# Kernel optimization log

Hardware: AMD Instinct MI355X
Metric: run time of the kernel (lower is better)

The kernel has to match this reference:

```python
import jax, jax.numpy as jnp
import numpy as np

N_HEADS = 16
D_EMBED = 1024
BATCH = 1
SEQ = 4096


def setup_inputs() -> dict:
    key = jax.random.key(0)
    ks = jax.random.split(key, 5)
    d = D_EMBED
    x = jax.random.normal(ks[0], (BATCH, SEQ, d), dtype=jnp.float32)
    # torch Linear weights stored as (in, out) so y = x @ W + b
    W_in = jax.random.normal(ks[1], (d, 3 * d), dtype=jnp.float32) / np.sqrt(d)
    b_in = jax.random.normal(ks[2], (3 * d,), dtype=jnp.float32) * 0.02
    W_out = jax.random.normal(ks[3], (d, d), dtype=jnp.float32) / np.sqrt(d)
    b_out = jax.random.normal(ks[4], (d,), dtype=jnp.float32) * 0.02
    return {"x": x, "W_in": W_in, "b_in": b_in, "W_out": W_out, "b_out": b_out}


def reference(x, W_in, b_in, W_out, b_out):
    B, S, d = x.shape
    H = N_HEADS
    dh = d // H
    qkv = x @ W_in + b_in                      # [B, S, 3d]
    q, k, v = jnp.split(qkv, 3, axis=-1)       # each [B, S, d]
    # [B, S, H, dh] -> [B, H, S, dh]
    q = q.reshape(B, S, H, dh).transpose(0, 2, 1, 3)
    k = k.reshape(B, S, H, dh).transpose(0, 2, 1, 3)
    v = v.reshape(B, S, H, dh).transpose(0, 2, 1, 3)
    scores = jnp.einsum("bhqd,bhkd->bhqk", q, k) / jnp.sqrt(jnp.float32(dh))
    causal = jnp.tril(jnp.ones((S, S), dtype=bool))  # True = keep
    scores = jnp.where(causal, scores, -jnp.inf)
    attn = jax.nn.softmax(scores, axis=-1)
    out = jnp.einsum("bhqk,bhkd->bhqd", attn, v)     # [B, H, S, dh]
    out = out.transpose(0, 2, 1, 3).reshape(B, S, d)
    return out @ W_out + b_out
```

## Files before the change

kernel.cpp:

```cpp
#include <hip/hip_runtime.h>
#include <stdint.h>

#define S_LEN 4096
#define D_EMB 1024
#define NH 16
#define DHEAD 64
#define N3 3072

typedef __attribute__((ext_vector_type(8))) short short8;
typedef __attribute__((ext_vector_type(4))) short short4v;
typedef __attribute__((ext_vector_type(4))) float f32x4;

#define OFF_XB    0u
#define OFF_WINT  4194304u
#define OFF_WOUTT 7340032u
#define OFF_Q     8388608u
#define OFF_ATTN  20971520u

#define QSCALE 0.1803368801111204f
#define DEFER_THR 11.0f

__device__ __forceinline__ unsigned short f2bf(float f) {
  unsigned u = __float_as_uint(f);
  unsigned r = u + 0x7FFFu + ((u >> 16) & 1u);
  return (unsigned short)(r >> 16);
}
__device__ __forceinline__ unsigned cvtpk_bf16(float lo, float hi) {
  unsigned r;
  asm("v_cvt_pk_bf16_f32 %0, %1, %2" : "=v"(r) : "v"(lo), "v"(hi));
  return r;
}
__device__ __forceinline__ void gload16(const void* g, void* l) {
  __builtin_amdgcn_global_load_lds((const __attribute__((address_space(1))) void*)g,
                                   (__attribute__((address_space(3))) void*)l, 16, 0, 0);
}

__global__ __launch_bounds__(256) void prep_kernel(const float* __restrict__ x,
                                                   const float* __restrict__ W_in,
                                                   const float* __restrict__ W_out,
                                                   ushort* __restrict__ xb,
                                                   ushort* __restrict__ wint,
                                                   ushort* __restrict__ woutt) {
  __shared__ float tile[32][65];
  int b = blockIdx.x;
  int tid = threadIdx.x;
  if (b < 4096) {
    int i = (b * 256 + tid) * 4;
    float4 v = *(const float4*)(x + i);
    ushort4 o;
    o.x = f2bf(v.x); o.y = f2bf(v.y); o.z = f2bf(v.z); o.w = f2bf(v.w);
    *(ushort4*)(xb + i) = o;
    return;
  }
  const float* src;
  ushort* dst;
  int C, bx, by;
  if (b < 5632) {
    int t = b - 4096;
    src = W_in; dst = wint; C = N3;
    bx = t % 48; by = t / 48;
  } else {
    int t = b - 5632;
    src = W_out; dst = woutt; C = D_EMB;
    bx = t & 15; by = t >> 4;
  }
  const int R = D_EMB;
  int r0 = by * 32, c0 = bx * 64;
  int lr = tid >> 3, lc8 = (tid & 7) * 8;
  float4 v0 = *(const float4*)&src[(size_t)(r0 + lr) * C + c0 + lc8];
  float4 v1 = *(const float4*)&src[(size_t)(r0 + lr) * C + c0 + lc8 + 4];
  tile[lr][lc8 + 0] = v0.x; tile[lr][lc8 + 1] = v0.y;
  tile[lr][lc8 + 2] = v0.z; tile[lr][lc8 + 3] = v0.w;
  tile[lr][lc8 + 4] = v1.x; tile[lr][lc8 + 5] = v1.y;
  tile[lr][lc8 + 6] = v1.z; tile[lr][lc8 + 7] = v1.w;
  __syncthreads();
  int oc = tid >> 2, q = tid & 3;
  short8 o;
#pragma unroll
  for (int i = 0; i < 8; ++i) o[i] = (short)f2bf(tile[q * 8 + i][oc]);
  *(short8*)&dst[(size_t)(c0 + oc) * R + r0 + q * 8] = o;
}

__global__ __launch_bounds__(512, 2) void gemm1_8phase(const ushort* __restrict__ A,
                                                       const ushort* __restrict__ Bt,
                                                       const float* __restrict__ bias,
                                                       ushort* __restrict__ o16) {
  __shared__ ushort L[57344];
  const int K = 1024;
  int tid = threadIdx.x, w = tid >> 6, lane = tid & 63;
  int wr = w >> 2, wc = w & 3;
  int l15 = lane & 15, g = lane >> 4;
  int lr = lane >> 3, lc = lane & 7;
  int swcol = (lc ^ lr) * 8;
  int rxor = (l15 & 7) << 3;
  int id = blockIdx.y * 16 + blockIdx.x;
  int id2 = (id & 7) * 32 + (id >> 3);
  int bm = (id2 >> 4) * 256, bn = (id2 & 15) * 192;

  f32x4 acc[8][3];
#pragma unroll
  for (int m = 0; m < 8; ++m)
#pragma unroll
    for (int n = 0; n < 3; ++n) acc[m][n] = (f32x4){0.f, 0.f, 0.f, 0.f};

  auto stageA = [&](int t, int h) {
#pragma unroll
    for (int r2 = 0; r2 < 2; ++r2)
      gload16(A + (size_t)(bm + h * 128 + r2 * 64 + w * 8 + lr) * K + t * 64 + swcol,
              &L[(t & 1) * 16384 + h * 8192 + r2 * 4096 + w * 512]);
  };
  auto stageB0 = [&](int t) {
#pragma unroll
    for (int r2 = 0; r2 < 2; ++r2)
      gload16(Bt + (size_t)(bn + r2 * 64 + w * 8 + lr) * K + t * 64 + swcol,
              &L[32768 + (t & 1) * 12288 + r2 * 4096 + w * 512]);
  };
  auto stageB1 = [&](int t) {
    gload16(Bt + (size_t)(bn + 128 + w * 8 + lr) * K + t * 64 + swcol,
            &L[32768 + (t & 1) * 12288 + 8192 + w * 512]);
  };

  short8 bf[3][2], af[2][2];
  auto readB = [&](int tb) {
    int base = 32768 + tb * 12288;
#pragma unroll
    for (int n = 0; n < 3; ++n)
#pragma unroll
      for (int ks = 0; ks < 2; ++ks)
        bf[n][ks] = *(const short8*)&L[base + (wc * 48 + n * 16 + l15) * 64 + ((ks * 32 + g * 8) ^ rxor)];
  };
  auto readA2 = [&](int tb, int m0) {
    int base = tb * 16384 + wr * 8192;
#pragma unroll
    for (int mi = 0; mi < 2; ++mi)
#pragma unroll
      for (int ks = 0; ks < 2; ++ks)
        af[mi][ks] = *(const short8*)&L[base + ((m0 + mi) * 16 + l15) * 64 + ((ks * 32 + g * 8) ^ rxor)];
  };
  auto mfma6 = [&](int m0) {
#pragma unroll
    for (int mi = 0; mi < 2; ++mi)
#pragma unroll
      for (int n = 0; n < 3; ++n)
#pragma unroll
        for (int ks = 0; ks < 2; ++ks)
          acc[m0 + mi][n] =
              __builtin_amdgcn_mfma_f32_16x16x32_bf16(af[mi][ks], bf[n][ks], acc[m0 + mi][n], 0, 0, 0);
  };

#define BAR() __builtin_amdgcn_s_barrier()
#define LGK0() asm volatile("s_waitcnt lgkmcnt(0)" ::: "memory")
#define VM3() asm volatile("s_waitcnt vmcnt(3)" ::: "memory")
#define VM0() asm volatile("s_waitcnt vmcnt(0)" ::: "memory")

  stageA(0, 0); stageA(0, 1); stageB0(0); stageB1(0);
  stageB0(1); stageB1(1);
  VM3();
  BAR();

  for (int i = 0; i < 8; ++i) {
    int T = 2 * i;
    bool more = (T + 2 < 16);
    readB(0); readA2(0, 0); stageA(T + 1, 0);
    BAR(); LGK0();
    __builtin_amdgcn_s_setprio(1); mfma6(0); __builtin_amdgcn_s_setprio(0);
    BAR();
    readA2(0, 2); stageA(T + 1, 1);
    BAR(); LGK0();
    __builtin_amdgcn_s_setprio(1); mfma6(2); __builtin_amdgcn_s_setprio(0);
    BAR();
    readA2(0, 4); if (more) stageB0(T + 2);
    BAR(); LGK0();
    __builtin_amdgcn_s_setprio(1); mfma6(4); __builtin_amdgcn_s_setprio(0);
    BAR();
    readA2(0, 6); if (more) stageB1(T + 2);
    BAR(); LGK0();
    __builtin_amdgcn_s_setprio(1); mfma6(6); __builtin_amdgcn_s_setprio(0);
    if (more) VM3(); else VM0();
    BAR();
    readB(1); readA2(1, 0); if (more) stageA(T + 2, 0);
    BAR(); LGK0();
    __builtin_amdgcn_s_setprio(1); mfma6(0); __builtin_amdgcn_s_setprio(0);
    BAR();
    readA2(1, 2); if (more) stageA(T + 2, 1);
    BAR(); LGK0();
    __builtin_amdgcn_s_setprio(1); mfma6(2); __builtin_amdgcn_s_setprio(0);
    BAR();
    readA2(1, 4); if (more) stageB0(T + 3);
    BAR(); LGK0();
    __builtin_amdgcn_s_setprio(1); mfma6(4); __builtin_amdgcn_s_setprio(0);
    BAR();
    readA2(1, 6); if (more) stageB1(T + 3);
    BAR(); LGK0();
    __builtin_amdgcn_s_setprio(1); mfma6(6); __builtin_amdgcn_s_setprio(0);
    if (more) VM3(); else VM0();
    BAR();
  }
#undef BAR
#undef LGK0
#undef VM3
#undef VM0

#pragma unroll
  for (int m = 0; m < 8; ++m) {
    int rbase = bm + wr * 128 + m * 16 + g * 4;
#pragma unroll
    for (int n = 0; n < 3; ++n) {
      int c = bn + wc * 48 + n * 16 + l15;
      float bv = bias[c];
      int which = c >> 10, cc = c & 1023, hh = cc >> 6, dcol = cc & 63;
      if (which == 2) {
        ushort4 o;
        o.x = f2bf(acc[m][n][0] + bv);
        o.y = f2bf(acc[m][n][1] + bv);
        o.z = f2bf(acc[m][n][2] + bv);
        o.w = f2bf(acc[m][n][3] + bv);
        *(ushort4*)&o16[8388608u + (size_t)hh * (DHEAD * (size_t)S_LEN) +
                        (size_t)dcol * S_LEN + rbase] = o;
      } else {
        float qs = (which == 0) ? QSCALE : 1.0f;
        ushort* dst = o16 + (size_t)which * 4194304u +
                      (size_t)hh * (S_LEN * DHEAD) + dcol;
#pragma unroll
        for (int j = 0; j < 4; ++j)
          dst[(size_t)(rbase + j) * DHEAD] = f2bf((acc[m][n][j] + bv) * qs);
      }
    }
  }
}

#define BK 64

__global__ __launch_bounds__(256) void gemm2_kernel(const ushort* __restrict__ A,
                                                    const ushort* __restrict__ Bt,
                                                    const float* __restrict__ bias,
                                                    float* __restrict__ o32,
                                                    int N, int K) {
  __shared__ ushort L[36864];
  int tid = threadIdx.x, w = tid >> 6, lane = tid & 63;
  int wr = w >> 1, wc = w & 1;
  int l15 = lane & 15, g = lane >> 4;
  int lr = lane >> 3, lc = lane & 7;
  int swcol = (lc ^ lr) * 8;
  int rxor = (l15 & 7) << 3;
  int gx = gridDim.x;
  int id = blockIdx.y * gx + blockIdx.x;
  int q8 = (gx * gridDim.y) >> 3;
  int id2 = (id & 7) * q8 + (id >> 3);
  int bm = (id2 / gx) * 128, bn = (id2 % gx) * 64;
  f32x4 acc[4][2];
#pragma unroll
  for (int m = 0; m < 4; ++m)
#pragma unroll
    for (int n = 0; n < 2; ++n) acc[m][n] = (f32x4){0.f, 0.f, 0.f, 0.f};

  auto stage = [&](int t) {
    int buf = t % 3;
#pragma unroll
    for (int i = 0; i < 4; ++i) {
      int ch = w * 4 + i;
      gload16(A + (size_t)(bm + ch * 8 + lr) * K + t * 64 + swcol,
              &L[buf * 8192 + ch * 512]);
    }
#pragma unroll
    for (int i = 0; i < 2; ++i) {
      int ch = w * 2 + i;
      gload16(Bt + (size_t)(bn + ch * 8 + lr) * K + t * 64 + swcol,
              &L[24576 + buf * 4096 + ch * 512]);
    }
  };

  const int NT = 16;
  stage(0); stage(1);
  asm volatile("s_waitcnt vmcnt(6)" ::: "memory");
  __builtin_amdgcn_s_barrier();

  for (int t = 0; t < NT; ++t) {
    int buf = t % 3;
    if (t + 2 < NT) stage(t + 2);
    const ushort* Ab = &L[buf * 8192];
    const ushort* Bb = &L[24576 + buf * 4096];
    short8 a[4][2], b[2][2];
#pragma unroll
    for (int m = 0; m < 4; ++m)
#pragma unroll
      for (int ks = 0; ks < 2; ++ks)
        a[m][ks] = *(const short8*)&Ab[(wr * 64 + m * 16 + l15) * 64 + ((ks * 32 + g * 8) ^ rxor)];
#pragma unroll
    for (int n = 0; n < 2; ++n)
#pragma unroll
      for (int ks = 0; ks < 2; ++ks)
        b[n][ks] = *(const short8*)&Bb[(wc * 32 + n * 16 + l15) * 64 + ((ks * 32 + g * 8) ^ rxor)];
    asm volatile("s_waitcnt lgkmcnt(0)" ::: "memory");
    __builtin_amdgcn_s_setprio(1);
#pragma unroll
    for (int m = 0; m < 4; ++m)
#pragma unroll
      for (int n = 0; n < 2; ++n)
#pragma unroll
        for (int ks = 0; ks < 2; ++ks)
          acc[m][n] = __builtin_amdgcn_mfma_f32_16x16x32_bf16(a[m][ks], b[n][ks], acc[m][n], 0, 0, 0);
    __builtin_amdgcn_s_setprio(0);
    if (t + 2 < NT)
      asm volatile("s_waitcnt vmcnt(6)" ::: "memory");
    else if (t + 1 < NT)
      asm volatile("s_waitcnt vmcnt(0)" ::: "memory");
    __builtin_amdgcn_s_barrier();
  }

#pragma unroll
  for (int m = 0; m < 4; ++m) {
    int rbase = bm + wr * 64 + m * 16 + g * 4;
#pragma unroll
    for (int n = 0; n < 2; ++n) {
      int c = bn + wc * 32 + n * 16 + l15;
      float bv = bias[c];
#pragma unroll
      for (int j = 0; j < 4; ++j)
        o32[(size_t)(rbase + j) * N + c] = acc[m][n][j] + bv;
    }
  }
}

__global__ __launch_bounds__(512) void attn_kernel(const ushort* __restrict__ Q,
                                                   const ushort* __restrict__ Kg,
                                                   const ushort* __restrict__ Vtg,
                                                   ushort* __restrict__ O) {
  __shared__ ushort Ks[2][64 * 64];
  __shared__ ushort Vs[2][64 * 64];
  int bid = blockIdx.x;
  int h = bid & 15;
  int qt = (bid < 256) ? (31 - (bid >> 4)) : ((bid - 256) >> 4);
  int q0 = qt * 128;
  int tid = threadIdx.x, w = tid >> 6, lane = tid & 63;
  int l15 = lane & 15, g = lane >> 4;
  const ushort* qh = Q + (size_t)h * (S_LEN * DHEAD);
  const ushort* kh = Kg + (size_t)h * (S_LEN * DHEAD);
  const ushort* vh = Vtg + (size_t)h * (DHEAD * (size_t)S_LEN);
  int srow = w * 8 + (lane >> 3);
  int sgcol = (((lane & 7) ^ ((lane >> 3) & 7))) * 8;
  ushort* kdst0 = &Ks[0][w * 512];  ushort* kdst1 = &Ks[1][w * 512];
  ushort* vdst0 = &Vs[0][w * 512];  ushort* vdst1 = &Vs[1][w * 512];
  int kxor = (l15 & 7) << 4;
  int koff0 = ((g * 16) ^ kxor) >> 1;
  int koff1 = ((64 + g * 16) ^ kxor) >> 1;
  int voff[4];
#pragma unroll
  for (int ct = 0; ct < 4; ++ct) voff[ct] = ((ct * 32 + g * 8) ^ kxor) >> 1;

  int qrow = q0 + w * 16 + l15;
  short8 aq[2];
#pragma unroll
  for (int t = 0; t < 2; ++t)
    aq[t] = *(const short8*)&qh[(size_t)qrow * DHEAD + t * 32 + g * 8];

  f32x4 acc_o[4];
#pragma unroll
  for (int dt = 0; dt < 4; ++dt) acc_o[dt] = (f32x4){0.f, 0.f, 0.f, 0.f};
  float m = -1e30f, l = 0.f;
  int last = 2 * qt + 1;

  gload16(&kh[(size_t)srow * DHEAD + sgcol], kdst0);
  gload16(&vh[(size_t)srow * S_LEN + sgcol], vdst0);
  asm volatile("s_waitcnt vmcnt(0)" ::: "memory");
  __syncthreads();
  int cur = 0;

  for (int it = 0; it <= last; ++it) {
    int kv0 = it * 64;
    bool more = (it < last);
    const ushort* Kc = Ks[cur];
    const ushort* Vc = Vs[cur];

    if (more) {
      int kv1 = kv0 + 64;
      gload16(&kh[(size_t)(kv1 + srow) * DHEAD + sgcol], cur ? kdst0 : kdst1);
      gload16(&vh[(size_t)srow * S_LEN + kv1 + sgcol], cur ? vdst0 : vdst1);
    }

    f32x4 accs[4];
#pragma unroll
    for (int ct = 0; ct < 4; ++ct) accs[ct] = (f32x4){0.f, 0.f, 0.f, 0.f};
    __builtin_amdgcn_s_setprio(1);
#pragma unroll
    for (int ct = 0; ct < 4; ++ct) {
      int rb = (ct * 16 + l15) * 64;
      short8 kf0 = *(const short8*)&Kc[rb + koff0];
      short8 kf1 = *(const short8*)&Kc[rb + koff1];
      accs[ct] = __builtin_amdgcn_mfma_f32_16x16x32_bf16(kf0, aq[0], accs[ct], 0, 0, 0);
      accs[ct] = __builtin_amdgcn_mfma_f32_16x16x32_bf16(kf1, aq[1], accs[ct], 0, 0, 0);
    }
    __builtin_amdgcn_s_setprio(0);

    if (it >= 2 * qt) {
#pragma unroll
      for (int ct = 0; ct < 4; ++ct) {
        int kbase = kv0 + ct * 16 + g * 4;
#pragma unroll
        for (int j = 0; j < 4; ++j)
          if (kbase + j > qrow) accs[ct][j] = -1e30f;
      }
    }

    float a0 = fmaxf(fmaxf(accs[0][0], accs[0][1]), fmaxf(accs[0][2], accs[0][3]));
    float a1 = fmaxf(fmaxf(accs[1][0], accs[1][1]), fmaxf(accs[1][2], accs[1][3]));
    float a2 = fmaxf(fmaxf(accs[2][0], accs[2][1]), fmaxf(accs[2][2], accs[2][3]));
    float a3 = fmaxf(fmaxf(accs[3][0], accs[3][1]), fmaxf(accs[3][2], accs[3][3]));
    float pm = fmaxf(fmaxf(a0, a1), fmaxf(a2, a3));

    if (!__all(pm <= m + DEFER_THR)) {
      pm = fmaxf(pm, __shfl_xor(pm, 16));
      pm = fmaxf(pm, __shfl_xor(pm, 32));
      float mnew = fmaxf(m, pm);
      float corr = __builtin_amdgcn_exp2f(m - mnew);
      l *= corr; m = mnew;
#pragma unroll
      for (int dt = 0; dt < 4; ++dt)
#pragma unroll
        for (int j = 0; j < 4; ++j) acc_o[dt][j] *= corr;
    }

    float rs = 0.f;
    short8 pk8[2];
#pragma unroll
    for (int t2 = 0; t2 < 2; ++t2) {
      float p0 = __builtin_amdgcn_exp2f(accs[2 * t2][0] - m);
      float p1 = __builtin_amdgcn_exp2f(accs[2 * t2][1] - m);
      float p2 = __builtin_amdgcn_exp2f(accs[2 * t2][2] - m);
      float p3 = __builtin_amdgcn_exp2f(accs[2 * t2][3] - m);
      float p4 = __builtin_amdgcn_exp2f(accs[2 * t2 + 1][0] - m);
      float p5 = __builtin_amdgcn_exp2f(accs[2 * t2 + 1][1] - m);
      float p6 = __builtin_amdgcn_exp2f(accs[2 * t2 + 1][2] - m);
      float p7 = __builtin_amdgcn_exp2f(accs[2 * t2 + 1][3] - m);
      rs += ((p0 + p1) + (p2 + p3)) + ((p4 + p5) + (p6 + p7));
      union { unsigned u[4]; short8 v; } pu;
      pu.u[0] = cvtpk_bf16(p0, p1);
      pu.u[1] = cvtpk_bf16(p2, p3);
      pu.u[2] = cvtpk_bf16(p4, p5);
      pu.u[3] = cvtpk_bf16(p6, p7);
      pk8[t2] = pu.v;
    }
    l += rs;

    __builtin_amdgcn_s_setprio(1);
#pragma unroll
    for (int dt = 0; dt < 4; ++dt) {
      int rb = (dt * 16 + l15) * 64;
#pragma unroll
      for (int t2 = 0; t2 < 2; ++t2) {
        union { short4v hh[2]; short8 v; } vu;
        vu.hh[0] = *(const short4v*)&Vc[rb + voff[2 * t2]];
        vu.hh[1] = *(const short4v*)&Vc[rb + voff[2 * t2 + 1]];
        acc_o[dt] = __builtin_amdgcn_mfma_f32_16x16x32_bf16(vu.v, pk8[t2], acc_o[dt], 0, 0, 0);
      }
    }
    __builtin_amdgcn_s_setprio(0);

    asm volatile("s_waitcnt vmcnt(0)" ::: "memory");
    __syncthreads();
    cur ^= 1;
  }

  l += __shfl_xor(l, 16);
  l += __shfl_xor(l, 32);
  float rl = (l > 0.f) ? 1.f / l : 0.f;
#pragma unroll
  for (int dt = 0; dt < 4; ++dt) {
    ushort4 o;
    o.x = f2bf(acc_o[dt][0] * rl);
    o.y = f2bf(acc_o[dt][1] * rl);
    o.z = f2bf(acc_o[dt][2] * rl);
    o.w = f2bf(acc_o[dt][3] * rl);
    *(ushort4*)&O[(size_t)qrow * D_EMB + h * DHEAD + dt * 16 + g * 4] = o;
  }
}

extern "C" void kernel_launch(void* const* d_in, const int* in_sizes, int n_in,
                              void* d_out, int out_size, void* d_ws, size_t ws_size,
                              hipStream_t stream) {
  const float* x = (const float*)d_in[0];
  const float* W_in = (const float*)d_in[1];
  const float* b_in = (const float*)d_in[2];
  const float* W_out = (const float*)d_in[3];
  const float* b_out = (const float*)d_in[4];
  float* out = (float*)d_out;
  ushort* ws = (ushort*)d_ws;

  prep_kernel<<<6144, 256, 0, stream>>>(x, W_in, W_out,
                                        ws + OFF_XB, ws + OFF_WINT, ws + OFF_WOUTT);
  gemm1_8phase<<<dim3(16, 16), 512, 0, stream>>>(
      ws + OFF_XB, ws + OFF_WINT, b_in, ws + OFF_Q);
  attn_kernel<<<512, 512, 0, stream>>>(
      ws + OFF_Q, ws + OFF_Q + 4194304u, ws + OFF_Q + 8388608u, ws + OFF_ATTN);
  gemm2_kernel<<<dim3(16, 32), 256, 0, stream>>>(
      ws + OFF_ATTN, ws + OFF_WOUTT, b_out, out, D_EMB, D_EMB);
}
```

Before: 120.2 us.

## Widen attention KV tile from 64 to 128 keys per iteration

```diff
diff --git a/kernel.cpp b/kernel.cpp
--- a/kernel.cpp
+++ b/kernel.cpp
@@ -326,8 +326,8 @@
                                                    const ushort* __restrict__ Kg,
                                                    const ushort* __restrict__ Vtg,
                                                    ushort* __restrict__ O) {
-  __shared__ ushort Ks[2][64 * 64];
-  __shared__ ushort Vs[2][64 * 64];
+  __shared__ ushort Ks[2][128 * 64];
+  __shared__ ushort Vs[2][64 * 128];
   int bid = blockIdx.x;
   int h = bid & 15;
   int qt = (bid < 256) ? (31 - (bid >> 4)) : ((bid - 256) >> 4);
@@ -337,16 +337,18 @@
   const ushort* qh = Q + (size_t)h * (S_LEN * DHEAD);
   const ushort* kh = Kg + (size_t)h * (S_LEN * DHEAD);
   const ushort* vh = Vtg + (size_t)h * (DHEAD * (size_t)S_LEN);
-  int srow = w * 8 + (lane >> 3);
-  int sgcol = (((lane & 7) ^ ((lane >> 3) & 7))) * 8;
-  ushort* kdst0 = &Ks[0][w * 512];  ushort* kdst1 = &Ks[1][w * 512];
-  ushort* vdst0 = &Vs[0][w * 512];  ushort* vdst1 = &Vs[1][w * 512];
+
+  int krow_l = lane >> 3;
+  int kcol = ((lane & 7) ^ krow_l) * 8;
+  int vrow_l = lane >> 4;
+  int vslot = lane & 15;
+
   int kxor = (l15 & 7) << 4;
   int koff0 = ((g * 16) ^ kxor) >> 1;
   int koff1 = ((64 + g * 16) ^ kxor) >> 1;
-  int voff[4];
-#pragma unroll
-  for (int ct = 0; ct < 4; ++ct) voff[ct] = ((ct * 32 + g * 8) ^ kxor) >> 1;
+  int voff[8];
+#pragma unroll
+  for (int ct = 0; ct < 8; ++ct) voff[ct] = ((ct * 32 + g * 8) ^ kxor) >> 1;
 
   int qrow = q0 + w * 16 + l15;
   short8 aq[2];
@@ -358,32 +360,41 @@
 #pragma unroll
   for (int dt = 0; dt < 4; ++dt) acc_o[dt] = (f32x4){0.f, 0.f, 0.f, 0.f};
   float m = -1e30f, l = 0.f;
-  int last = 2 * qt + 1;
-
-  gload16(&kh[(size_t)srow * DHEAD + sgcol], kdst0);
-  gload16(&vh[(size_t)srow * S_LEN + sgcol], vdst0);
+  int last = qt;
+
+  auto stageKV = [&](int kv, int buf) {
+#pragma unroll
+    for (int hh2 = 0; hh2 < 2; ++hh2) {
+      int krow = w * 16 + hh2 * 8 + krow_l;
+      gload16(&kh[(size_t)(kv + krow) * DHEAD + kcol], &Ks[buf][w * 1024 + hh2 * 512]);
+    }
+#pragma unroll
+    for (int hh2 = 0; hh2 < 2; ++hh2) {
+      int d = w * 8 + hh2 * 4 + vrow_l;
+      int vcol = (vslot ^ (d & 7)) * 8;
+      gload16(&vh[(size_t)d * S_LEN + kv + vcol], &Vs[buf][w * 1024 + hh2 * 512]);
+    }
+  };
+
+  stageKV(0, 0);
   asm volatile("s_waitcnt vmcnt(0)" ::: "memory");
   __syncthreads();
   int cur = 0;
 
   for (int it = 0; it <= last; ++it) {
-    int kv0 = it * 64;
+    int kv0 = it * 128;
     bool more = (it < last);
     const ushort* Kc = Ks[cur];
     const ushort* Vc = Vs[cur];
 
-    if (more) {
-      int kv1 = kv0 + 64;
-      gload16(&kh[(size_t)(kv1 + srow) * DHEAD + sgcol], cur ? kdst0 : kdst1);
-      gload16(&vh[(size_t)srow * S_LEN + kv1 + sgcol], cur ? vdst0 : vdst1);
-    }
-
-    f32x4 accs[4];
-#pragma unroll
-    for (int ct = 0; ct < 4; ++ct) accs[ct] = (f32x4){0.f, 0.f, 0.f, 0.f};
+    if (more) stageKV(kv0 + 128, cur ^ 1);
+
+    f32x4 accs[8];
+#pragma unroll
+    for (int ct = 0; ct < 8; ++ct) accs[ct] = (f32x4){0.f, 0.f, 0.f, 0.f};
     __builtin_amdgcn_s_setprio(1);
 #pragma unroll
-    for (int ct = 0; ct < 4; ++ct) {
+    for (int ct = 0; ct < 8; ++ct) {
       int rb = (ct * 16 + l15) * 64;
       short8 kf0 = *(const short8*)&Kc[rb + koff0];
       short8 kf1 = *(const short8*)&Kc[rb + koff1];
@@ -392,9 +403,9 @@
     }
     __builtin_amdgcn_s_setprio(0);
 
-    if (it >= 2 * qt) {
-#pragma unroll
-      for (int ct = 0; ct < 4; ++ct) {
+    if (it == qt) {
+#pragma unroll
+      for (int ct = 0; ct < 8; ++ct) {
         int kbase = kv0 + ct * 16 + g * 4;
 #pragma unroll
         for (int j = 0; j < 4; ++j)
@@ -402,11 +413,16 @@
       }
     }
 
-    float a0 = fmaxf(fmaxf(accs[0][0], accs[0][1]), fmaxf(accs[0][2], accs[0][3]));
-    float a1 = fmaxf(fmaxf(accs[1][0], accs[1][1]), fmaxf(accs[1][2], accs[1][3]));
-    float a2 = fmaxf(fmaxf(accs[2][0], accs[2][1]), fmaxf(accs[2][2], accs[2][3]));
-    float a3 = fmaxf(fmaxf(accs[3][0], accs[3][1]), fmaxf(accs[3][2], accs[3][3]));
-    float pm = fmaxf(fmaxf(a0, a1), fmaxf(a2, a3));
+    float t0 = fmaxf(fmaxf(accs[0][0], accs[0][1]), fmaxf(accs[0][2], accs[0][3]));
+    float t1 = fmaxf(fmaxf(accs[1][0], accs[1][1]), fmaxf(accs[1][2], accs[1][3]));
+    float t2m = fmaxf(fmaxf(accs[2][0], accs[2][1]), fmaxf(accs[2][2], accs[2][3]));
+    float t3 = fmaxf(fmaxf(accs[3][0], accs[3][1]), fmaxf(accs[3][2], accs[3][3]));
+    float t4 = fmaxf(fmaxf(accs[4][0], accs[4][1]), fmaxf(accs[4][2], accs[4][3]));
+    float t5 = fmaxf(fmaxf(accs[5][0], accs[5][1]), fmaxf(accs[5][2], accs[5][3]));
+    float t6 = fmaxf(fmaxf(accs[6][0], accs[6][1]), fmaxf(accs[6][2], accs[6][3]));
+    float t7 = fmaxf(fmaxf(accs[7][0], accs[7][1]), fmaxf(accs[7][2], accs[7][3]));
+    float pm = fmaxf(fmaxf(fmaxf(t0, t1), fmaxf(t2m, t3)),
+                     fmaxf(fmaxf(t4, t5), fmaxf(t6, t7)));
 
     if (!__all(pm <= m + DEFER_THR)) {
       pm = fmaxf(pm, __shfl_xor(pm, 16));
@@ -421,9 +437,9 @@
     }
 
     float rs = 0.f;
-    short8 pk8[2];
-#pragma unroll
-    for (int t2 = 0; t2 < 2; ++t2) {
+    short8 pk8[4];
+#pragma unroll
+    for (int t2 = 0; t2 < 4; ++t2) {
       float p0 = __builtin_amdgcn_exp2f(accs[2 * t2][0] - m);
       float p1 = __builtin_amdgcn_exp2f(accs[2 * t2][1] - m);
       float p2 = __builtin_amdgcn_exp2f(accs[2 * t2][2] - m);
@@ -445,9 +461,9 @@
     __builtin_amdgcn_s_setprio(1);
 #pragma unroll
     for (int dt = 0; dt < 4; ++dt) {
-      int rb = (dt * 16 + l15) * 64;
-#pragma unroll
-      for (int t2 = 0; t2 < 2; ++t2) {
+      int rb = (dt * 16 + l15) * 128;
+#pragma unroll
+      for (int t2 = 0; t2 < 4; ++t2) {
         union { short4v hh[2]; short8 v; } vu;
         vu.hh[0] = *(const short4v*)&Vc[rb + voff[2 * t2]];
         vu.hh[1] = *(const short4v*)&Vc[rb + voff[2 * t2 + 1]];
```

Measured after the change: 145.4 us. 1.21x slower.
